# Performance work log

Measured on AMD Instinct MI355X. Metric: run time of the kernel, lower is better.

Reference implementation:

```python
import jax, jax.numpy as jnp
import numpy as np

B, S, D, H = 4, 4096, 1024, 16
LOCAL_W, GLOBAL_W = 128, 1024


def _mha_window(x, w_in, b_in, w_out, b_out, window, n_heads):
    # Faithful port of sliding_window_attention + nn.MultiheadAttention self-attn.
    b, s, d = x.shape
    nw = (s + window - 1) // window
    pad = nw * window - s
    xp = jnp.pad(x, ((0, 0), (0, pad), (0, 0))) if pad > 0 else x
    xw = xp.reshape(b * nw, window, d)                      # [b*nw, w, d]
    qkv = xw @ w_in.T + b_in                                # [b*nw, w, 3d]
    q, k, v = jnp.split(qkv, 3, axis=-1)
    dh = d // n_heads
    q = q.reshape(-1, window, n_heads, dh)
    k = k.reshape(-1, window, n_heads, dh)
    v = v.reshape(-1, window, n_heads, dh)
    # NOTE: torch code passes a FLOAT triu(ones) mask -> it is ADDED to logits
    # (adds +1.0 above the diagonal), not -inf causal masking. Replicated exactly.
    add_mask = jnp.triu(jnp.ones((window, window), dtype=x.dtype), k=1)
    scores = jnp.einsum('bqhd,bkhd->bhqk', q, k) / np.sqrt(dh).astype(x.dtype)
    scores = scores + add_mask
    attn = jax.nn.softmax(scores, axis=-1)
    o = jnp.einsum('bhqk,bkhd->bqhd', attn, v).reshape(-1, window, d)
    o = o @ w_out.T + b_out
    return o.reshape(b, nw * window, d)[:, :s, :]


def setup_inputs() -> dict:
    key = jax.random.key(0)
    ks = jax.random.split(key, 10)
    sc = 0.02
    inp = {
        'lqs': jax.random.normal(ks[0], (B, S, D), jnp.float32),
        'gqs': jax.random.normal(ks[1], (B, S, D), jnp.float32),
        'wl_in': jax.random.normal(ks[2], (3 * D, D), jnp.float32) * sc,
        'bl_in': jnp.zeros((3 * D,), jnp.float32),
        'wl_out': jax.random.normal(ks[3], (D, D), jnp.float32) * sc,
        'bl_out': jnp.zeros((D,), jnp.float32),
        'wg_in': jax.random.normal(ks[4], (3 * D, D), jnp.float32) * sc,
        'bg_in': jnp.zeros((3 * D,), jnp.float32),
        'wg_out': jax.random.normal(ks[5], (D, D), jnp.float32) * sc,
        'bg_out': jnp.zeros((D,), jnp.float32),
    }
    return inp


def reference(lqs, gqs, wl_in, bl_in, wl_out, bl_out, wg_in, bg_in, wg_out, bg_out):
    local_out = _mha_window(lqs, wl_in, bl_in, wl_out, bl_out, LOCAL_W, H)
    global_out = _mha_window(gqs, wg_in, bg_in, wg_out, bg_out, GLOBAL_W, H)
    return (local_out, global_out)
```

## Files before the change

kernel.cpp:

```cpp
#include <hip/hip_runtime.h>
#include <stdint.h>

typedef short v8s __attribute__((ext_vector_type(8)));
typedef float v4f __attribute__((ext_vector_type(4)));

__device__ __forceinline__ unsigned short f2bf(float f) {
    union { float f; uint32_t u; } x; x.f = f;
    uint32_t r = (x.u + 0x7fffu + ((x.u >> 16) & 1u)) >> 16;
    return (unsigned short)r;
}
__device__ __forceinline__ uint32_t cvt_pk_bf16(float lo, float hi) {
    uint32_t r;
    asm("v_cvt_pk_bf16_f32 %0, %1, %2" : "=v"(r) : "v"(lo), "v"(hi));
    return r;
}

#define QSCALE 0.18033688011112042f
#define L2E    1.4426950408889634f

__global__ __launch_bounds__(256) void cast_f32_bf16(const float* __restrict__ in,
                                                     unsigned short* __restrict__ out, int n) {
    int i = (blockIdx.x * 256 + threadIdx.x) * 4;
    const int stride = gridDim.x * 256 * 4;
    for (; i < n; i += stride) {
        float4 v = *(const float4*)(in + i);
        ushort4 o;
        o.x = f2bf(v.x); o.y = f2bf(v.y); o.z = f2bf(v.z); o.w = f2bf(v.w);
        *(ushort4*)(out + i) = o;
    }
}

template <bool OUT_F32, bool VSPLIT>
__global__ __launch_bounds__(256) void gemm_nt(const unsigned short* __restrict__ A,
                                               const unsigned short* __restrict__ B,
                                               const float* __restrict__ bias,
                                               void* __restrict__ Cout,
                                               unsigned short* __restrict__ vt,
                                               int M, int N, int K, int ldc) {
    __shared__ unsigned short As[128 * 64];
    __shared__ unsigned short Bs[128 * 64];
    const int tid = threadIdx.x;
    const int wv = tid >> 6, lane = tid & 63;
    const int quad = lane >> 4, l16 = lane & 15;
    const int tiles_n = N >> 7;
    const int tm = blockIdx.x / tiles_n, tn = blockIdx.x - tm * tiles_n;
    const int m0 = tm << 7, n0 = tn << 7;
    const int wr = (wv >> 1) * 64, wc = (wv & 1) * 64;

    v4f acc[4][4] = {};

    for (int k0 = 0; k0 < K; k0 += 64) {
        __syncthreads();
#pragma unroll
        for (int j = 0; j < 4; ++j) {
            const int cb = (wv * 4 + j) * 64;
            const int cl = cb + lane;
            const int row = cl >> 3;
            const int kc = (cl & 7) ^ (row & 7);
            const unsigned short* ga = A + (size_t)(m0 + row) * K + k0 + kc * 8;
            const unsigned short* gb = B + (size_t)(n0 + row) * K + k0 + kc * 8;
            __builtin_amdgcn_global_load_lds(
                (const __attribute__((address_space(1))) unsigned int*)ga,
                (__attribute__((address_space(3))) unsigned int*)(As + cb * 8), 16, 0, 0);
            __builtin_amdgcn_global_load_lds(
                (const __attribute__((address_space(1))) unsigned int*)gb,
                (__attribute__((address_space(3))) unsigned int*)(Bs + cb * 8), 16, 0, 0);
        }
        __syncthreads();
#pragma unroll
        for (int ks = 0; ks < 2; ++ks) {
            v8s af[4], bf[4];
#pragma unroll
            for (int mt = 0; mt < 4; ++mt) {
                const int row = wr + mt * 16 + l16;
                const int ch = row * 8 + ((ks * 4 + quad) ^ (row & 7));
                af[mt] = *(const v8s*)(As + ch * 8);
            }
#pragma unroll
            for (int nt = 0; nt < 4; ++nt) {
                const int row = wc + nt * 16 + l16;
                const int ch = row * 8 + ((ks * 4 + quad) ^ (row & 7));
                bf[nt] = *(const v8s*)(Bs + ch * 8);
            }
#pragma unroll
            for (int mt = 0; mt < 4; ++mt)
#pragma unroll
                for (int nt = 0; nt < 4; ++nt)
                    acc[mt][nt] = __builtin_amdgcn_mfma_f32_16x16x32_bf16(
                        af[mt], bf[nt], acc[mt][nt], 0, 0, 0);
        }
    }
#pragma unroll
    for (int nt = 0; nt < 4; ++nt) {
        const int col = n0 + wc + nt * 16 + l16;
        const float bv = bias[col];
        if (VSPLIT && col >= 2048) {
#pragma unroll
            for (int mt = 0; mt < 4; ++mt) {
                const int rowb = m0 + wr + mt * 16 + quad * 4;
                ushort4 o;
                o.x = f2bf(acc[mt][nt][0] + bv);
                o.y = f2bf(acc[mt][nt][1] + bv);
                o.z = f2bf(acc[mt][nt][2] + bv);
                o.w = f2bf(acc[mt][nt][3] + bv);
                *(ushort4*)(vt + (size_t)(col - 2048) * M + rowb) = o;
            }
        } else {
            const float scl = (VSPLIT && col < 1024) ? QSCALE : 1.0f;
#pragma unroll
            for (int mt = 0; mt < 4; ++mt) {
                const int rowb = m0 + wr + mt * 16 + quad * 4;
#pragma unroll
                for (int r = 0; r < 4; ++r) {
                    if (OUT_F32)
                        ((float*)Cout)[(size_t)(rowb + r) * ldc + col] = acc[mt][nt][r] + bv;
                    else
                        ((unsigned short*)Cout)[(size_t)(rowb + r) * ldc + col] =
                            f2bf((acc[mt][nt][r] + bv) * scl);
                }
            }
        }
    }
}

__global__ __launch_bounds__(256, 3) void attn_win(const unsigned short* __restrict__ qk,
                                                   const unsigned short* __restrict__ Vt,
                                                   unsigned short* __restrict__ O,
                                                   int W) {
    const int nkt = W >> 7;
    const int tid = threadIdx.x, wv = tid >> 6, lane = tid & 63;
    const int quad = lane >> 4, l16 = lane & 15;

    int wh, qb;
    if (nkt == 8) {
        const int g = blockIdx.x;
        wh = (g >> 6) * 8 + (g & 7);
        qb = (g >> 3) & 7;
    } else {
        wh = blockIdx.x; qb = 0;
    }
    const int winst = wh >> 4, head = wh & 15;
    const size_t rw = (size_t)winst * W;

    __shared__ unsigned short Ks[128 * 64];
    __shared__ unsigned short Vs[64 * 128];
    __shared__ unsigned short Ps[4 * 16 * 136];
    unsigned short* Pw = Ps + wv * 16 * 136;

    v8s qf[2][2];
#pragma unroll
    for (int st = 0; st < 2; ++st) {
        const size_t qrow = rw + (size_t)(qb * 128 + wv * 32 + st * 16 + l16);
        const unsigned short* qp = qk + qrow * 2048 + head * 64 + quad * 8;
        qf[st][0] = *(const v8s*)qp;
        qf[st][1] = *(const v8s*)(qp + 32);
    }

    float rsum[2] = {0.f, 0.f};
    v4f oacc[2][4] = {};

    for (int kt = 0; kt < nkt; ++kt) {
        __syncthreads();
#pragma unroll
        for (int j = 0; j < 4; ++j) {
            const int cb = (wv * 4 + j) * 64;
            const int cl = cb + lane;
            const int key = cl >> 3, c = cl & 7;
            const unsigned short* src = qk + (rw + (size_t)(kt * 128 + key)) * 2048
                                        + 1024 + head * 64 + ((c ^ (key & 7)) * 8);
            __builtin_amdgcn_global_load_lds(
                (const __attribute__((address_space(1))) unsigned int*)src,
                (__attribute__((address_space(3))) unsigned int*)(Ks + cb * 8), 16, 0, 0);
        }
#pragma unroll
        for (int j = 0; j < 4; ++j) {
            const int cb = (wv * 4 + j) * 64;
            const int cl = cb + lane;
            const int dh = cl >> 4, c = cl & 15;
            const unsigned short* src = Vt + (size_t)(head * 64 + dh) * 16384
                                        + rw + (size_t)(kt * 128) + ((c ^ (dh & 7)) * 8);
            __builtin_amdgcn_global_load_lds(
                (const __attribute__((address_space(1))) unsigned int*)src,
                (__attribute__((address_space(3))) unsigned int*)(Vs + cb * 8), 16, 0, 0);
        }
        __syncthreads();

        v4f sf[2][8] = {};
#pragma unroll
        for (int nt = 0; nt < 8; ++nt) {
            const int krow = nt * 16 + l16;
#pragma unroll
            for (int ks = 0; ks < 2; ++ks) {
                const v8s kf = *(const v8s*)(Ks + krow * 64 + ((ks * 4 + quad) ^ (krow & 7)) * 8);
                sf[0][nt] = __builtin_amdgcn_mfma_f32_16x16x32_bf16(kf, qf[0][ks], sf[0][nt], 0, 0, 0);
                sf[1][nt] = __builtin_amdgcn_mfma_f32_16x16x32_bf16(kf, qf[1][ks], sf[1][nt], 0, 0, 0);
            }
        }

#pragma unroll
        for (int st = 0; st < 2; ++st) {
            const int irow = qb * 128 + wv * 32 + st * 16 + l16;
            float rl = 0.f;
#pragma unroll
            for (int nt = 0; nt < 8; ++nt) {
                const int jb = kt * 128 + nt * 16 + quad * 4;
                float e[4];
#pragma unroll
                for (int r = 0; r < 4; ++r)
                    e[r] = exp2f(sf[st][nt][r] + ((jb + r > irow) ? L2E : 0.0f));
                rl += (e[0] + e[1]) + (e[2] + e[3]);
                uint2 pk;
                pk.x = cvt_pk_bf16(e[0], e[1]);
                pk.y = cvt_pk_bf16(e[2], e[3]);
                *(uint2*)(Pw + l16 * 136 + nt * 16 + quad * 4) = pk;
            }
            rsum[st] += rl;
#pragma unroll
            for (int kk = 0; kk < 4; ++kk) {
                const v8s pf = *(const v8s*)(Pw + l16 * 136 + kk * 32 + quad * 8);
#pragma unroll
                for (int dt = 0; dt < 4; ++dt) {
                    const int dh = dt * 16 + l16;
                    const v8s vf = *(const v8s*)(Vs + dh * 128 + ((kk * 4 + quad) ^ (dh & 7)) * 8);
                    oacc[st][dt] = __builtin_amdgcn_mfma_f32_16x16x32_bf16(pf, vf, oacc[st][dt], 0, 0, 0);
                }
            }
        }
    }

#pragma unroll
    for (int st = 0; st < 2; ++st) {
        float l = rsum[st];
        l += __shfl_xor(l, 16);
        l += __shfl_xor(l, 32);
        const float inv = 1.0f / l;
#pragma unroll
        for (int r = 0; r < 4; ++r) {
            const float invr = __shfl(inv, quad * 4 + r);
            const size_t row = rw + (size_t)(qb * 128 + wv * 32 + st * 16 + quad * 4 + r);
#pragma unroll
            for (int dt = 0; dt < 4; ++dt)
                O[row * 1024 + head * 64 + dt * 16 + l16] = f2bf(oacc[st][dt][r] * invr);
        }
    }
}

extern "C" void kernel_launch(void* const* d_in, const int* in_sizes, int n_in,
                              void* d_out, int out_size, void* d_ws, size_t ws_size,
                              hipStream_t stream) {
    const float* lqs    = (const float*)d_in[0];
    const float* gqs    = (const float*)d_in[1];
    const float* wl_in  = (const float*)d_in[2];
    const float* bl_in  = (const float*)d_in[3];
    const float* wl_out = (const float*)d_in[4];
    const float* bl_out = (const float*)d_in[5];
    const float* wg_in  = (const float*)d_in[6];
    const float* bg_in  = (const float*)d_in[7];
    const float* wg_out = (const float*)d_in[8];
    const float* bg_out = (const float*)d_in[9];

    char* ws = (char*)d_ws;
    unsigned short* Xbf    = (unsigned short*)(ws);
    unsigned short* Obf    = (unsigned short*)(ws + 33554432);
    unsigned short* Winbf  = (unsigned short*)(ws + 67108864);
    unsigned short* Woutbf = (unsigned short*)(ws + 73400320);
    unsigned short* QKbf   = (unsigned short*)(ws + 75497472);
    unsigned short* Vtbf   = (unsigned short*)(ws + 142606336);

    const int R = 4 * 4096;
    const int D = 1024;

    for (int path = 0; path < 2; ++path) {
        const float* x     = path == 0 ? lqs : gqs;
        const float* w_in  = path == 0 ? wl_in : wg_in;
        const float* b_in  = path == 0 ? bl_in : bg_in;
        const float* w_out = path == 0 ? wl_out : wg_out;
        const float* b_out = path == 0 ? bl_out : bg_out;
        const int W        = path == 0 ? 128 : 1024;
        float* outp = (float*)d_out + (size_t)path * R * D;

        hipLaunchKernelGGL(cast_f32_bf16, dim3(4096), dim3(256), 0, stream, x, Xbf, R * D);
        hipLaunchKernelGGL(cast_f32_bf16, dim3(3072), dim3(256), 0, stream, w_in, Winbf, 3 * D * D);
        hipLaunchKernelGGL(cast_f32_bf16, dim3(1024), dim3(256), 0, stream, w_out, Woutbf, D * D);
        hipLaunchKernelGGL((gemm_nt<false, true>), dim3(128 * 24), dim3(256), 0, stream,
                           Xbf, Winbf, b_in, (void*)QKbf, Vtbf, R, 3 * D, D, 2048);
        hipLaunchKernelGGL(attn_win, dim3(2048), dim3(256), 0, stream, QKbf, Vtbf, Obf, W);
        hipLaunchKernelGGL((gemm_nt<true, false>), dim3(128 * 8), dim3(256), 0, stream,
                           Obf, Woutbf, b_out, (void*)outp, (unsigned short*)nullptr,
                           R, D, D, 1024);
    }
}
```

Baseline: 751.3 us.

## Switch attention kernel to 32x32x16 MFMA and keep P in registers

Result: faster. 703.9 us (-6.3%).

```diff
diff --git a/kernel.cpp b/kernel.cpp
--- a/kernel.cpp
+++ b/kernel.cpp
@@ -3,6 +3,7 @@
 
 typedef short v8s __attribute__((ext_vector_type(8)));
 typedef float v4f __attribute__((ext_vector_type(4)));
+typedef float f32x16 __attribute__((ext_vector_type(16)));
 
 __device__ __forceinline__ unsigned short f2bf(float f) {
     union { float f; uint32_t u; } x; x.f = f;
@@ -129,7 +130,7 @@
                                                    int W) {
     const int nkt = W >> 7;
     const int tid = threadIdx.x, wv = tid >> 6, lane = tid & 63;
-    const int quad = lane >> 4, l16 = lane & 15;
+    const int hi = lane >> 5, l32 = lane & 31;
 
     int wh, qb;
     if (nkt == 8) {
@@ -144,20 +145,20 @@
 
     __shared__ unsigned short Ks[128 * 64];
     __shared__ unsigned short Vs[64 * 128];
-    __shared__ unsigned short Ps[4 * 16 * 136];
-    unsigned short* Pw = Ps + wv * 16 * 136;
-
-    v8s qf[2][2];
-#pragma unroll
-    for (int st = 0; st < 2; ++st) {
-        const size_t qrow = rw + (size_t)(qb * 128 + wv * 32 + st * 16 + l16);
-        const unsigned short* qp = qk + qrow * 2048 + head * 64 + quad * 8;
-        qf[st][0] = *(const v8s*)qp;
-        qf[st][1] = *(const v8s*)(qp + 32);
-    }
-
-    float rsum[2] = {0.f, 0.f};
-    v4f oacc[2][4] = {};
+
+    const int irow = qb * 128 + wv * 32 + l32;
+    const int thr  = irow - 4 * hi;
+
+    v8s qf[4];
+    {
+        const size_t qrow = rw + (size_t)irow;
+        const unsigned short* qp = qk + qrow * 2048 + head * 64 + hi * 8;
+#pragma unroll
+        for (int ks = 0; ks < 4; ++ks) qf[ks] = *(const v8s*)(qp + ks * 16);
+    }
+
+    float rsum = 0.f;
+    f32x16 oacc[2] = {};
 
     for (int kt = 0; kt < nkt; ++kt) {
         __syncthreads();
@@ -185,63 +186,57 @@
         }
         __syncthreads();
 
-        v4f sf[2][8] = {};
-#pragma unroll
-        for (int nt = 0; nt < 8; ++nt) {
-            const int krow = nt * 16 + l16;
-#pragma unroll
-            for (int ks = 0; ks < 2; ++ks) {
-                const v8s kf = *(const v8s*)(Ks + krow * 64 + ((ks * 4 + quad) ^ (krow & 7)) * 8);
-                sf[0][nt] = __builtin_amdgcn_mfma_f32_16x16x32_bf16(kf, qf[0][ks], sf[0][nt], 0, 0, 0);
-                sf[1][nt] = __builtin_amdgcn_mfma_f32_16x16x32_bf16(kf, qf[1][ks], sf[1][nt], 0, 0, 0);
-            }
-        }
-
-#pragma unroll
-        for (int st = 0; st < 2; ++st) {
-            const int irow = qb * 128 + wv * 32 + st * 16 + l16;
-            float rl = 0.f;
-#pragma unroll
-            for (int nt = 0; nt < 8; ++nt) {
-                const int jb = kt * 128 + nt * 16 + quad * 4;
-                float e[4];
-#pragma unroll
-                for (int r = 0; r < 4; ++r)
-                    e[r] = exp2f(sf[st][nt][r] + ((jb + r > irow) ? L2E : 0.0f));
-                rl += (e[0] + e[1]) + (e[2] + e[3]);
-                uint2 pk;
-                pk.x = cvt_pk_bf16(e[0], e[1]);
-                pk.y = cvt_pk_bf16(e[2], e[3]);
-                *(uint2*)(Pw + l16 * 136 + nt * 16 + quad * 4) = pk;
-            }
-            rsum[st] += rl;
-#pragma unroll
-            for (int kk = 0; kk < 4; ++kk) {
-                const v8s pf = *(const v8s*)(Pw + l16 * 136 + kk * 32 + quad * 8);
-#pragma unroll
-                for (int dt = 0; dt < 4; ++dt) {
-                    const int dh = dt * 16 + l16;
-                    const v8s vf = *(const v8s*)(Vs + dh * 128 + ((kk * 4 + quad) ^ (dh & 7)) * 8);
-                    oacc[st][dt] = __builtin_amdgcn_mfma_f32_16x16x32_bf16(pf, vf, oacc[st][dt], 0, 0, 0);
+#pragma unroll
+        for (int kg = 0; kg < 4; ++kg) {
+            f32x16 s = {};
+            const int key0 = kg * 32 + l32;
+#pragma unroll
+            for (int ks = 0; ks < 4; ++ks) {
+                const v8s kf = *(const v8s*)(Ks + key0 * 64
+                                             + (((ks << 1) | hi) ^ (key0 & 7)) * 8);
+                s = __builtin_amdgcn_mfma_f32_32x32x16_bf16(kf, qf[ks], s, 0, 0, 0);
+            }
+            const int kb = kt * 128 + kg * 32;
+            float e[16];
+#pragma unroll
+            for (int r = 0; r < 16; ++r) {
+                const int kx = kb + (r & 3) + 8 * (r >> 2);
+                e[r] = __builtin_amdgcn_exp2f(s[r] + ((kx > thr) ? L2E : 0.0f));
+            }
+            rsum += (((e[0] + e[1]) + (e[2] + e[3])) + ((e[4] + e[5]) + (e[6] + e[7])))
+                  + (((e[8] + e[9]) + (e[10] + e[11])) + ((e[12] + e[13]) + (e[14] + e[15])));
+#pragma unroll
+            for (int h = 0; h < 2; ++h) {
+                uint32_t wA = cvt_pk_bf16(e[8 * h + 0], e[8 * h + 1]);
+                uint32_t wB = cvt_pk_bf16(e[8 * h + 4], e[8 * h + 5]);
+                uint32_t wC = cvt_pk_bf16(e[8 * h + 2], e[8 * h + 3]);
+                uint32_t wD = cvt_pk_bf16(e[8 * h + 6], e[8 * h + 7]);
+                asm("v_permlane32_swap_b32 %0, %1" : "+v"(wA), "+v"(wB));
+                asm("v_permlane32_swap_b32 %0, %1" : "+v"(wC), "+v"(wD));
+                union { uint32_t u[4]; v8s s8; } pa;
+                pa.u[0] = wA; pa.u[1] = wC; pa.u[2] = wB; pa.u[3] = wD;
+                const int c0 = kg * 4 + h * 2 + hi;
+#pragma unroll
+                for (int dhg = 0; dhg < 2; ++dhg) {
+                    const int dh = dhg * 32 + l32;
+                    const v8s vf = *(const v8s*)(Vs + dh * 128 + ((c0 ^ (dh & 7))) * 8);
+                    oacc[dhg] = __builtin_amdgcn_mfma_f32_32x32x16_bf16(
+                        pa.s8, vf, oacc[dhg], 0, 0, 0);
                 }
             }
         }
     }
 
-#pragma unroll
-    for (int st = 0; st < 2; ++st) {
-        float l = rsum[st];
-        l += __shfl_xor(l, 16);
-        l += __shfl_xor(l, 32);
-        const float inv = 1.0f / l;
-#pragma unroll
-        for (int r = 0; r < 4; ++r) {
-            const float invr = __shfl(inv, quad * 4 + r);
-            const size_t row = rw + (size_t)(qb * 128 + wv * 32 + st * 16 + quad * 4 + r);
-#pragma unroll
-            for (int dt = 0; dt < 4; ++dt)
-                O[row * 1024 + head * 64 + dt * 16 + l16] = f2bf(oacc[st][dt][r] * invr);
-        }
+    const float tot = rsum + __shfl_xor(rsum, 32);
+    const float inv = 1.0f / tot;
+#pragma unroll
+    for (int r = 0; r < 16; ++r) {
+        const int q32 = (r & 3) + 8 * (r >> 2) + 4 * hi;
+        const float invr = __shfl(inv, q32 + (hi << 5));
+        const size_t row = rw + (size_t)(qb * 128 + wv * 32 + q32);
+#pragma unroll
+        for (int dhg = 0; dhg < 2; ++dhg)
+            O[row * 1024 + head * 64 + dhg * 32 + l32] = f2bf(oacc[dhg][r] * invr);
     }
 }
 
```
